# Kernel optimization log

Measured on AMD Instinct MI355X. Metric: run time of the kernel, lower is better.

Reference implementation:

```python
import jax, jax.numpy as jnp
import numpy as np

IMAGE_SIZE = 512
STRIDES = (8, 16, 32)
W_SEG, W_DET, W_CLS = 1.0, 1.0, 0.5


def _bce_logits(x, y):
    # numerically stable binary cross entropy with logits (broadcasts y)
    return jnp.maximum(x, 0.0) - x * y + jnp.log1p(jnp.exp(-jnp.abs(x)))


def _focal_loss_mean(logits, targets, num_classes, alpha=0.25, gamma=2.0):
    # sigmoid focal loss; targets are class indices, -1 (or any negative) => all-background row
    t = jax.nn.one_hot(targets, num_classes, dtype=logits.dtype)
    p = jax.nn.sigmoid(logits)
    ce = _bce_logits(logits, t)
    p_t = p * t + (1.0 - p) * (1.0 - t)
    a_t = alpha * t + (1.0 - alpha) * (1.0 - t)
    return jnp.mean(a_t * (1.0 - p_t) ** gamma * ce)


def _det_scale_loss(cls_logits, reg_preds, cent_preds, boxes, labels, stride):
    B, Cp1, H, W = cls_logits.shape
    C = Cp1 - 1
    L = H * W
    cls = jnp.transpose(cls_logits, (0, 2, 3, 1))[..., 1:].reshape(B, L, C)
    reg = jnp.transpose(reg_preds, (0, 2, 3, 1)).reshape(B, L, 4)
    cent = cent_preds.reshape(B, L)
    xs = (jnp.arange(W, dtype=jnp.float32) + 0.5) * stride
    ys = (jnp.arange(H, dtype=jnp.float32) + 0.5) * stride
    gy, gx = jnp.meshgrid(ys, xs, indexing='ij')
    loc_x = gx.reshape(-1)
    loc_y = gy.reshape(-1)

    def per_image(cls_i, reg_i, cent_i, gb, gl):
        b = gb * IMAGE_SIZE  # [cx,cy,w,h] in pixels
        x0 = b[:, 0] - b[:, 2] * 0.5
        y0 = b[:, 1] - b[:, 3] * 0.5
        x1 = b[:, 0] + b[:, 2] * 0.5
        y1 = b[:, 1] + b[:, 3] * 0.5
        l = loc_x[:, None] - x0[None, :]
        t = loc_y[:, None] - y0[None, :]
        r = x1[None, :] - loc_x[:, None]
        btm = y1[None, :] - loc_y[:, None]
        ltrb = jnp.stack([l, t, r, btm], axis=-1)  # (L, N, 4)
        inside = jnp.min(ltrb, axis=-1) > 0
        area = (x1 - x0) * (y1 - y0)
        masked_area = jnp.where(inside, area[None, :], jnp.inf)
        idx = jnp.argmin(masked_area, axis=-1)  # min-area matched box per location
        pos = jnp.any(inside, axis=-1)
        cls_t = jnp.where(pos, gl[idx], -1)
        reg_t = jnp.take_along_axis(ltrb, idx[:, None, None], axis=1)[:, 0, :] / stride
        lr = reg_t[:, jnp.array([0, 2])]
        tb = reg_t[:, jnp.array([1, 3])]
        eps = 1e-6
        cen_t = jnp.sqrt(jnp.clip((jnp.min(lr, -1) / (jnp.max(lr, -1) + eps)) * (jnp.min(tb, -1) / (jnp.max(tb, -1) + eps)), 0.0, 1.0))
        cls_l = _focal_loss_mean(cls_i, cls_t, C)
        npos = jnp.sum(pos)
        d = reg_i - reg_t
        sl1 = jnp.mean(jnp.where(jnp.abs(d) < 1.0, 0.5 * d * d, jnp.abs(d) - 0.5), axis=-1)
        posf = pos.astype(jnp.float32)
        denom = jnp.maximum(npos, 1).astype(jnp.float32)
        reg_l = jnp.where(npos > 0, jnp.sum(sl1 * posf) / denom, 0.0)
        bce = _bce_logits(cent_i, cen_t)
        cen_l = jnp.where(npos > 0, jnp.sum(bce * posf) / denom, 0.0)
        return cls_l, reg_l, cen_l

    cl, rl, cel = jax.vmap(per_image)(cls, reg, cent, boxes, labels)
    return jnp.mean(cl), jnp.mean(rl), jnp.mean(cel)


def _total_loss(seg_logits, seg_mask, cls_list, reg_list, cen_list, boxes, labels, cls_pred, cls_target):
    # segmentation: BCE-with-logits, integer mask broadcast as float target over channels
    seg_t = seg_mask.astype(jnp.float32)[:, None, :, :]  # (B,1,H,W) broadcasts vs (B,C,H,W)
    seg_loss = jnp.mean(_bce_logits(seg_logits, seg_t))
    tot_cls = 0.0
    tot_reg = 0.0
    tot_cen = 0.0
    for s in range(3):
        cl, rl, cel = _det_scale_loss(cls_list[s], reg_list[s], cen_list[s], boxes, labels, STRIDES[s])
        tot_cls = tot_cls + cl
        tot_reg = tot_reg + rl
        tot_cen = tot_cen + cel
    n = 3.0
    det_loss = tot_cls / n + tot_reg / n + tot_cen / n
    cls_loss = _focal_loss_mean(cls_pred, cls_target, cls_pred.shape[-1])
    return W_SEG * seg_loss + W_DET * det_loss + W_CLS * cls_loss


def setup_inputs() -> dict:
    key = jax.random.key(0)
    ks = jax.random.split(key, 16)
    B = 32
    inp = {
        'seg_logits': jax.random.normal(ks[0], (B, 4, 512, 512), jnp.float32),
        'seg_mask': jax.random.randint(ks[1], (B, 512, 512), 0, 4, jnp.int32),
        'cls_logits_s0': jax.random.normal(ks[2], (B, 5, 64, 64), jnp.float32),
        'cls_logits_s1': jax.random.normal(ks[3], (B, 5, 32, 32), jnp.float32),
        'cls_logits_s2': jax.random.normal(ks[4], (B, 5, 16, 16), jnp.float32),
        'reg_preds_s0': jax.random.normal(ks[5], (B, 4, 64, 64), jnp.float32),
        'reg_preds_s1': jax.random.normal(ks[6], (B, 4, 32, 32), jnp.float32),
        'reg_preds_s2': jax.random.normal(ks[7], (B, 4, 16, 16), jnp.float32),
        'centerness_s0': jax.random.normal(ks[8], (B, 1, 64, 64), jnp.float32),
        'centerness_s1': jax.random.normal(ks[9], (B, 1, 32, 32), jnp.float32),
        'centerness_s2': jax.random.normal(ks[10], (B, 1, 16, 16), jnp.float32),
        'boxes': jax.random.uniform(ks[11], (B, 20, 4), jnp.float32),
        'labels': jax.random.randint(ks[12], (B, 20), 0, 4, jnp.int32),
        'cls_pred': jax.random.normal(ks[13], (B, 10), jnp.float32),
        'cls_target': jax.random.randint(ks[14], (B,), 0, 10, jnp.int32),
    }
    return inp


def reference(seg_logits, seg_mask, cls_logits_s0, cls_logits_s1, cls_logits_s2, reg_preds_s0, reg_preds_s1, reg_preds_s2, centerness_s0, centerness_s1, centerness_s2, boxes, labels, cls_pred, cls_target):
    return _total_loss(seg_logits, seg_mask,
                       (cls_logits_s0, cls_logits_s1, cls_logits_s2),
                       (reg_preds_s0, reg_preds_s1, reg_preds_s2),
                       (centerness_s0, centerness_s1, centerness_s2),
                       boxes, labels, cls_pred, cls_target)
```

## Files before the change

### kernel.cpp

```cpp
#include <hip/hip_runtime.h>
#include <math.h>

#define NB 32
#define SEG_BLOCKS 2048


__device__ __forceinline__ float bce_logits(float x, float y) {
    float a = fabsf(x);
    return fmaxf(x, 0.f) - x * y + __logf(1.f + __expf(-a));
}

__device__ __forceinline__ float focal_elt(float x, float t) {
    float p = 1.f / (1.f + __expf(-x));
    float ce = bce_logits(x, t);
    float p_t = (t > 0.5f) ? p : (1.f - p);
    float a_t = (t > 0.5f) ? 0.25f : 0.75f;
    float om = 1.f - p_t;
    return a_t * om * om * ce;
}

template <int N>
__device__ void blk_reduce_arr(float* v) {
    __shared__ float sm[N][4];
    int lane = threadIdx.x & 63;
    int wid  = threadIdx.x >> 6;
#pragma unroll
    for (int j = 0; j < N; j++) {
        float x = v[j];
#pragma unroll
        for (int off = 32; off > 0; off >>= 1) x += __shfl_down(x, off, 64);
        if (lane == 0) sm[j][wid] = x;
    }
    __syncthreads();
    if (threadIdx.x == 0) {
#pragma unroll
        for (int j = 0; j < N; j++) {
            float s = 0.f;
#pragma unroll
            for (int w = 0; w < 4; w++) s += sm[j][w];
            v[j] = s;
        }
    }
}


__global__ __launch_bounds__(256) void seg_kernel(
        const float* __restrict__ logits, const int* __restrict__ mask,
        float* __restrict__ partial) {
    const int HW  = 512 * 512;
    const int QPI = HW / 4;
    const int TOTQ = NB * QPI;
    int tid = blockIdx.x * 256 + threadIdx.x;
    float acc = 0.f;
    for (int q = tid; q < TOTQ; q += SEG_BLOCKS * 256) {
        int b   = q >> 16;
        int hwq = q & 65535;
        const int4 m4 = ((const int4*)(mask + (size_t)b * HW))[hwq];
        float ty0 = (float)m4.x, ty1 = (float)m4.y, ty2 = (float)m4.z, ty3 = (float)m4.w;
        const float4* base = (const float4*)(logits + (size_t)b * 4 * HW);
#pragma unroll
        for (int c = 0; c < 4; c++) {
            float4 x4 = base[c * QPI + hwq];
            acc += bce_logits(x4.x, ty0) + bce_logits(x4.y, ty1)
                 + bce_logits(x4.z, ty2) + bce_logits(x4.w, ty3);
        }
    }
    float v[1] = {acc};
    blk_reduce_arr<1>(v);
    if (threadIdx.x == 0) partial[blockIdx.x] = v[0];
}


__global__ __launch_bounds__(256) void det_kernel(
        const float* __restrict__ cls0, const float* __restrict__ cls1, const float* __restrict__ cls2,
        const float* __restrict__ reg0, const float* __restrict__ reg1, const float* __restrict__ reg2,
        const float* __restrict__ cen0, const float* __restrict__ cen1, const float* __restrict__ cen2,
        const float* __restrict__ boxes, const int* __restrict__ labels,
        float* __restrict__ outws) {
    const int b = blockIdx.x;
    const int s = blockIdx.y;
    int Wd, shift, L; float stride;
    const float *cls, *reg, *cen;
    if (s == 0)      { Wd = 64; shift = 6; L = 4096; stride = 8.f;  cls = cls0; reg = reg0; cen = cen0; }
    else if (s == 1) { Wd = 32; shift = 5; L = 1024; stride = 16.f; cls = cls1; reg = reg1; cen = cen1; }
    else             { Wd = 16; shift = 4; L = 256;  stride = 32.f; cls = cls2; reg = reg2; cen = cen2; }

    __shared__ float sx0[20], sy0[20], sx1[20], sy1[20], sar[20];
    __shared__ int   slb[20];
    if (threadIdx.x < 20) {
        int k = threadIdx.x;
        const float* bb = boxes + (b * 20 + k) * 4;
        float cx = bb[0] * 512.f, cy = bb[1] * 512.f;
        float w  = bb[2] * 512.f, h  = bb[3] * 512.f;
        float x0 = cx - 0.5f * w, y0 = cy - 0.5f * h;
        float x1 = cx + 0.5f * w, y1 = cy + 0.5f * h;
        sx0[k] = x0; sy0[k] = y0; sx1[k] = x1; sy1[k] = y1;
        sar[k] = (x1 - x0) * (y1 - y0);
        slb[k] = labels[b * 20 + k];
    }
    __syncthreads();

    const float* clsb = cls + (size_t)b * 5 * L;
    const float* regb = reg + (size_t)b * 4 * L;
    const float* cenb = cen + (size_t)b * L;
    const float inv = 1.f / stride;

    float cls_s = 0.f, reg_s = 0.f, cen_s = 0.f, np = 0.f;
    for (int l = threadIdx.x; l < L; l += 256) {
        float lx = ((l & (Wd - 1)) + 0.5f) * stride;
        float ly = ((l >> shift)   + 0.5f) * stride;
        int bk = -1; float ba = INFINITY;
        float bl = 0.f, btp = 0.f, brr = 0.f, bbt = 0.f;
#pragma unroll
        for (int k = 0; k < 20; k++) {
            float li = lx - sx0[k], ti = ly - sy0[k];
            float ri = sx1[k] - lx, bi = sy1[k] - ly;
            float mn = fminf(fminf(li, ti), fminf(ri, bi));
            if (mn > 0.f && sar[k] < ba) {
                ba = sar[k]; bk = k;
                bl = li; btp = ti; brr = ri; bbt = bi;
            }
        }
        int tl = (bk >= 0) ? slb[bk] : -1;
#pragma unroll
        for (int c = 0; c < 4; c++) {
            float x = clsb[(c + 1) * L + l];
            cls_s += focal_elt(x, (c == tl) ? 1.f : 0.f);
        }
        if (bk >= 0) {
            float r0 = bl * inv, r1 = btp * inv, r2 = brr * inv, r3 = bbt * inv;
            float d0 = regb[0 * L + l] - r0;
            float d1 = regb[1 * L + l] - r1;
            float d2 = regb[2 * L + l] - r2;
            float d3 = regb[3 * L + l] - r3;
            float a0 = fabsf(d0), a1 = fabsf(d1), a2 = fabsf(d2), a3 = fabsf(d3);
            float sl = (a0 < 1.f ? 0.5f * d0 * d0 : a0 - 0.5f)
                     + (a1 < 1.f ? 0.5f * d1 * d1 : a1 - 0.5f)
                     + (a2 < 1.f ? 0.5f * d2 * d2 : a2 - 0.5f)
                     + (a3 < 1.f ? 0.5f * d3 * d3 : a3 - 0.5f);
            reg_s += 0.25f * sl;
            float mnlr = fminf(r0, r2), mxlr = fmaxf(r0, r2);
            float mntb = fminf(r1, r3), mxtb = fmaxf(r1, r3);
            float v = (mnlr / (mxlr + 1e-6f)) * (mntb / (mxtb + 1e-6f));
            v = fminf(fmaxf(v, 0.f), 1.f);
            float ct = sqrtf(v);
            cen_s += bce_logits(cenb[l], ct);
            np += 1.f;
        }
    }

    float v4[4] = {cls_s, reg_s, cen_s, np};
    blk_reduce_arr<4>(v4);
    if (threadIdx.x == 0) {
        float* o = outws + (size_t)(s * NB + b) * 4;
        o[0] = v4[0]; o[1] = v4[1]; o[2] = v4[2]; o[3] = v4[3];
    }
}


__global__ __launch_bounds__(256) void final_kernel(
        const float* __restrict__ segpart, const float* __restrict__ detws,
        const float* __restrict__ cls_pred, const int* __restrict__ cls_target,
        float* __restrict__ out) {
    float segs = 0.f;
    for (int i = threadIdx.x; i < SEG_BLOCKS; i += 256) segs += segpart[i];
    float clss = 0.f;
    for (int e = threadIdx.x; e < NB * 10; e += 256) {
        int i = e / 10, c = e - i * 10;
        clss += focal_elt(cls_pred[e], (cls_target[i] == c) ? 1.f : 0.f);
    }
    float v2[2] = {segs, clss};
    blk_reduce_arr<2>(v2);
    if (threadIdx.x == 0) {
        float seg_loss = v2[0] / 33554432.f;
        float cls_loss = v2[1] / 320.f;
        const int Ls[3] = {4096, 1024, 256};
        float tc = 0.f, tr = 0.f, tn = 0.f;
        for (int s = 0; s < 3; s++) {
            float ac = 0.f, ar = 0.f, an = 0.f;
            for (int i = 0; i < NB; i++) {
                const float* o = detws + (size_t)(s * NB + i) * 4;
                ac += o[0] / (Ls[s] * 4.f);
                float np = o[3];
                float denom = fmaxf(np, 1.f);
                if (np > 0.f) {
                    ar += o[1] / denom;
                    an += o[2] / denom;
                }
            }
            tc += ac / (float)NB;
            tr += ar / (float)NB;
            tn += an / (float)NB;
        }
        float det_loss = (tc + tr + tn) / 3.f;
        out[0] = seg_loss + det_loss + 0.5f * cls_loss;
    }
}


extern "C" void kernel_launch(void* const* d_in, const int* in_sizes, int n_in,
                              void* d_out, int out_size, void* d_ws, size_t ws_size,
                              hipStream_t stream) {
    const float* seg_logits = (const float*)d_in[0];
    const int*   seg_mask   = (const int*)d_in[1];
    const float* cls0 = (const float*)d_in[2];
    const float* cls1 = (const float*)d_in[3];
    const float* cls2 = (const float*)d_in[4];
    const float* reg0 = (const float*)d_in[5];
    const float* reg1 = (const float*)d_in[6];
    const float* reg2 = (const float*)d_in[7];
    const float* cen0 = (const float*)d_in[8];
    const float* cen1 = (const float*)d_in[9];
    const float* cen2 = (const float*)d_in[10];
    const float* boxes  = (const float*)d_in[11];
    const int*   labels = (const int*)d_in[12];
    const float* cls_pred   = (const float*)d_in[13];
    const int*   cls_target = (const int*)d_in[14];

    float* ws      = (float*)d_ws;
    float* segpart = ws;
    float* detws   = ws + SEG_BLOCKS;

    seg_kernel<<<SEG_BLOCKS, 256, 0, stream>>>(seg_logits, seg_mask, segpart);
    det_kernel<<<dim3(NB, 3), 256, 0, stream>>>(cls0, cls1, cls2,
                                                reg0, reg1, reg2,
                                                cen0, cen1, cen2,
                                                boxes, labels, detws);
    final_kernel<<<1, 256, 0, stream>>>(segpart, detws, cls_pred, cls_target,
                                        (float*)d_out);
}
```

Measured before the change: 288.2 us.

## Fuse detection loss into segmentation kernel and simplify final reduction

The detection loss work moves into the first 96 blocks of the segmentation kernel. Those blocks also run their share of the segmentation grid-stride loop, so one launch is removed and the small det workload overlaps the bandwidth-bound seg pass. Each det block now computes its normalized per-scale loss directly, which reduces the final kernel to a single scalar block reduction. The cost is extra work and shared-memory pressure on the first blocks, plus a slightly different floating-point summation order.

```diff
diff --git a/kernel.cpp b/kernel.cpp
--- a/kernel.cpp
+++ b/kernel.cpp
@@ -3,6 +3,7 @@
 
 #define NB 32
 #define SEG_BLOCKS 2048
+#define DET_BLOCKS 96
 
 
 __device__ __forceinline__ float bce_logits(float x, float y) {
@@ -44,9 +45,100 @@
 }
 
 
-__global__ __launch_bounds__(256) void seg_kernel(
-        const float* __restrict__ logits, const int* __restrict__ mask,
-        float* __restrict__ partial) {
+__global__ __launch_bounds__(256) void fused_kernel(
+        const float* __restrict__ seg_logits, const int* __restrict__ mask,
+        const float* __restrict__ cls0, const float* __restrict__ cls1, const float* __restrict__ cls2,
+        const float* __restrict__ reg0, const float* __restrict__ reg1, const float* __restrict__ reg2,
+        const float* __restrict__ cen0, const float* __restrict__ cen1, const float* __restrict__ cen2,
+        const float* __restrict__ boxes, const int* __restrict__ labels,
+        float* __restrict__ segpart, float* __restrict__ detc) {
+
+    if (blockIdx.x < DET_BLOCKS) {
+        const int s = blockIdx.x >> 5;
+        const int b = blockIdx.x & 31;
+        int Wd, shift, L; float stride;
+        const float *cls, *reg, *cen;
+        if (s == 0)      { Wd = 64; shift = 6; L = 4096; stride = 8.f;  cls = cls0; reg = reg0; cen = cen0; }
+        else if (s == 1) { Wd = 32; shift = 5; L = 1024; stride = 16.f; cls = cls1; reg = reg1; cen = cen1; }
+        else             { Wd = 16; shift = 4; L = 256;  stride = 32.f; cls = cls2; reg = reg2; cen = cen2; }
+
+        __shared__ float sx0[20], sy0[20], sx1[20], sy1[20], sar[20];
+        __shared__ int   slb[20];
+        if (threadIdx.x < 20) {
+            int k = threadIdx.x;
+            const float* bb = boxes + (b * 20 + k) * 4;
+            float cx = bb[0] * 512.f, cy = bb[1] * 512.f;
+            float w  = bb[2] * 512.f, h  = bb[3] * 512.f;
+            float x0 = cx - 0.5f * w, y0 = cy - 0.5f * h;
+            float x1 = cx + 0.5f * w, y1 = cy + 0.5f * h;
+            sx0[k] = x0; sy0[k] = y0; sx1[k] = x1; sy1[k] = y1;
+            sar[k] = (x1 - x0) * (y1 - y0);
+            slb[k] = labels[b * 20 + k];
+        }
+        __syncthreads();
+
+        const float* clsb = cls + (size_t)b * 5 * L;
+        const float* regb = reg + (size_t)b * 4 * L;
+        const float* cenb = cen + (size_t)b * L;
+        const float inv = 1.f / stride;
+
+        float cls_s = 0.f, reg_s = 0.f, cen_s = 0.f, np = 0.f;
+        for (int l = threadIdx.x; l < L; l += 256) {
+            float lx = ((l & (Wd - 1)) + 0.5f) * stride;
+            float ly = ((l >> shift)   + 0.5f) * stride;
+            int bk = -1; float ba = INFINITY;
+            float bl = 0.f, btp = 0.f, brr = 0.f, bbt = 0.f;
+#pragma unroll
+            for (int k = 0; k < 20; k++) {
+                float li = lx - sx0[k], ti = ly - sy0[k];
+                float ri = sx1[k] - lx, bi = sy1[k] - ly;
+                float mn = fminf(fminf(li, ti), fminf(ri, bi));
+                if (mn > 0.f && sar[k] < ba) {
+                    ba = sar[k]; bk = k;
+                    bl = li; btp = ti; brr = ri; bbt = bi;
+                }
+            }
+            int tl = (bk >= 0) ? slb[bk] : -1;
+#pragma unroll
+            for (int c = 0; c < 4; c++) {
+                float x = clsb[(c + 1) * L + l];
+                cls_s += focal_elt(x, (c == tl) ? 1.f : 0.f);
+            }
+            if (bk >= 0) {
+                float r0 = bl * inv, r1 = btp * inv, r2 = brr * inv, r3 = bbt * inv;
+                float d0 = regb[0 * L + l] - r0;
+                float d1 = regb[1 * L + l] - r1;
+                float d2 = regb[2 * L + l] - r2;
+                float d3 = regb[3 * L + l] - r3;
+                float a0 = fabsf(d0), a1 = fabsf(d1), a2 = fabsf(d2), a3 = fabsf(d3);
+                float sl = (a0 < 1.f ? 0.5f * d0 * d0 : a0 - 0.5f)
+                         + (a1 < 1.f ? 0.5f * d1 * d1 : a1 - 0.5f)
+                         + (a2 < 1.f ? 0.5f * d2 * d2 : a2 - 0.5f)
+                         + (a3 < 1.f ? 0.5f * d3 * d3 : a3 - 0.5f);
+                reg_s += 0.25f * sl;
+                float mnlr = fminf(r0, r2), mxlr = fmaxf(r0, r2);
+                float mntb = fminf(r1, r3), mxtb = fmaxf(r1, r3);
+                float v = (mnlr / (mxlr + 1e-6f)) * (mntb / (mxtb + 1e-6f));
+                v = fminf(fmaxf(v, 0.f), 1.f);
+                float ct = sqrtf(v);
+                cen_s += bce_logits(cenb[l], ct);
+                np += 1.f;
+            }
+        }
+
+        float v4[4] = {cls_s, reg_s, cen_s, np};
+        blk_reduce_arr<4>(v4);
+        if (threadIdx.x == 0) {
+            float cls_l = v4[0] / (L * 4.f);
+            float npos  = v4[3];
+            float denom = fmaxf(npos, 1.f);
+            float reg_l = (npos > 0.f) ? v4[1] / denom : 0.f;
+            float cen_l = (npos > 0.f) ? v4[2] / denom : 0.f;
+            detc[blockIdx.x] = (cls_l + reg_l + cen_l) * (1.f / (float)DET_BLOCKS);
+        }
+        __syncthreads();
+    }
+
     const int HW  = 512 * 512;
     const int QPI = HW / 4;
     const int TOTQ = NB * QPI;
@@ -57,7 +149,7 @@
         int hwq = q & 65535;
         const int4 m4 = ((const int4*)(mask + (size_t)b * HW))[hwq];
         float ty0 = (float)m4.x, ty1 = (float)m4.y, ty2 = (float)m4.z, ty3 = (float)m4.w;
-        const float4* base = (const float4*)(logits + (size_t)b * 4 * HW);
+        const float4* base = (const float4*)(seg_logits + (size_t)b * 4 * HW);
 #pragma unroll
         for (int c = 0; c < 4; c++) {
             float4 x4 = base[c * QPI + hwq];
@@ -67,134 +159,26 @@
     }
     float v[1] = {acc};
     blk_reduce_arr<1>(v);
-    if (threadIdx.x == 0) partial[blockIdx.x] = v[0];
-}
-
-
-__global__ __launch_bounds__(256) void det_kernel(
-        const float* __restrict__ cls0, const float* __restrict__ cls1, const float* __restrict__ cls2,
-        const float* __restrict__ reg0, const float* __restrict__ reg1, const float* __restrict__ reg2,
-        const float* __restrict__ cen0, const float* __restrict__ cen1, const float* __restrict__ cen2,
-        const float* __restrict__ boxes, const int* __restrict__ labels,
-        float* __restrict__ outws) {
-    const int b = blockIdx.x;
-    const int s = blockIdx.y;
-    int Wd, shift, L; float stride;
-    const float *cls, *reg, *cen;
-    if (s == 0)      { Wd = 64; shift = 6; L = 4096; stride = 8.f;  cls = cls0; reg = reg0; cen = cen0; }
-    else if (s == 1) { Wd = 32; shift = 5; L = 1024; stride = 16.f; cls = cls1; reg = reg1; cen = cen1; }
-    else             { Wd = 16; shift = 4; L = 256;  stride = 32.f; cls = cls2; reg = reg2; cen = cen2; }
-
-    __shared__ float sx0[20], sy0[20], sx1[20], sy1[20], sar[20];
-    __shared__ int   slb[20];
-    if (threadIdx.x < 20) {
-        int k = threadIdx.x;
-        const float* bb = boxes + (b * 20 + k) * 4;
-        float cx = bb[0] * 512.f, cy = bb[1] * 512.f;
-        float w  = bb[2] * 512.f, h  = bb[3] * 512.f;
-        float x0 = cx - 0.5f * w, y0 = cy - 0.5f * h;
-        float x1 = cx + 0.5f * w, y1 = cy + 0.5f * h;
-        sx0[k] = x0; sy0[k] = y0; sx1[k] = x1; sy1[k] = y1;
-        sar[k] = (x1 - x0) * (y1 - y0);
-        slb[k] = labels[b * 20 + k];
-    }
-    __syncthreads();
-
-    const float* clsb = cls + (size_t)b * 5 * L;
-    const float* regb = reg + (size_t)b * 4 * L;
-    const float* cenb = cen + (size_t)b * L;
-    const float inv = 1.f / stride;
-
-    float cls_s = 0.f, reg_s = 0.f, cen_s = 0.f, np = 0.f;
-    for (int l = threadIdx.x; l < L; l += 256) {
-        float lx = ((l & (Wd - 1)) + 0.5f) * stride;
-        float ly = ((l >> shift)   + 0.5f) * stride;
-        int bk = -1; float ba = INFINITY;
-        float bl = 0.f, btp = 0.f, brr = 0.f, bbt = 0.f;
-#pragma unroll
-        for (int k = 0; k < 20; k++) {
-            float li = lx - sx0[k], ti = ly - sy0[k];
-            float ri = sx1[k] - lx, bi = sy1[k] - ly;
-            float mn = fminf(fminf(li, ti), fminf(ri, bi));
-            if (mn > 0.f && sar[k] < ba) {
-                ba = sar[k]; bk = k;
-                bl = li; btp = ti; brr = ri; bbt = bi;
-            }
-        }
-        int tl = (bk >= 0) ? slb[bk] : -1;
-#pragma unroll
-        for (int c = 0; c < 4; c++) {
-            float x = clsb[(c + 1) * L + l];
-            cls_s += focal_elt(x, (c == tl) ? 1.f : 0.f);
-        }
-        if (bk >= 0) {
-            float r0 = bl * inv, r1 = btp * inv, r2 = brr * inv, r3 = bbt * inv;
-            float d0 = regb[0 * L + l] - r0;
-            float d1 = regb[1 * L + l] - r1;
-            float d2 = regb[2 * L + l] - r2;
-            float d3 = regb[3 * L + l] - r3;
-            float a0 = fabsf(d0), a1 = fabsf(d1), a2 = fabsf(d2), a3 = fabsf(d3);
-            float sl = (a0 < 1.f ? 0.5f * d0 * d0 : a0 - 0.5f)
-                     + (a1 < 1.f ? 0.5f * d1 * d1 : a1 - 0.5f)
-                     + (a2 < 1.f ? 0.5f * d2 * d2 : a2 - 0.5f)
-                     + (a3 < 1.f ? 0.5f * d3 * d3 : a3 - 0.5f);
-            reg_s += 0.25f * sl;
-            float mnlr = fminf(r0, r2), mxlr = fmaxf(r0, r2);
-            float mntb = fminf(r1, r3), mxtb = fmaxf(r1, r3);
-            float v = (mnlr / (mxlr + 1e-6f)) * (mntb / (mxtb + 1e-6f));
-            v = fminf(fmaxf(v, 0.f), 1.f);
-            float ct = sqrtf(v);
-            cen_s += bce_logits(cenb[l], ct);
-            np += 1.f;
-        }
-    }
-
-    float v4[4] = {cls_s, reg_s, cen_s, np};
-    blk_reduce_arr<4>(v4);
-    if (threadIdx.x == 0) {
-        float* o = outws + (size_t)(s * NB + b) * 4;
-        o[0] = v4[0]; o[1] = v4[1]; o[2] = v4[2]; o[3] = v4[3];
-    }
+    if (threadIdx.x == 0) segpart[blockIdx.x] = v[0];
 }
 
 
 __global__ __launch_bounds__(256) void final_kernel(
-        const float* __restrict__ segpart, const float* __restrict__ detws,
+        const float* __restrict__ segpart, const float* __restrict__ detc,
         const float* __restrict__ cls_pred, const int* __restrict__ cls_target,
         float* __restrict__ out) {
-    float segs = 0.f;
-    for (int i = threadIdx.x; i < SEG_BLOCKS; i += 256) segs += segpart[i];
-    float clss = 0.f;
+    const float seg_scale = 1.f / 33554432.f;
+    const float cls_scale = 0.5f / 320.f;
+    float acc = 0.f;
+    for (int i = threadIdx.x; i < SEG_BLOCKS; i += 256) acc += segpart[i] * seg_scale;
+    if (threadIdx.x < DET_BLOCKS) acc += detc[threadIdx.x];
     for (int e = threadIdx.x; e < NB * 10; e += 256) {
         int i = e / 10, c = e - i * 10;
-        clss += focal_elt(cls_pred[e], (cls_target[i] == c) ? 1.f : 0.f);
-    }
-    float v2[2] = {segs, clss};
-    blk_reduce_arr<2>(v2);
-    if (threadIdx.x == 0) {
-        float seg_loss = v2[0] / 33554432.f;
-        float cls_loss = v2[1] / 320.f;
-        const int Ls[3] = {4096, 1024, 256};
-        float tc = 0.f, tr = 0.f, tn = 0.f;
-        for (int s = 0; s < 3; s++) {
-            float ac = 0.f, ar = 0.f, an = 0.f;
-            for (int i = 0; i < NB; i++) {
-                const float* o = detws + (size_t)(s * NB + i) * 4;
-                ac += o[0] / (Ls[s] * 4.f);
-                float np = o[3];
-                float denom = fmaxf(np, 1.f);
-                if (np > 0.f) {
-                    ar += o[1] / denom;
-                    an += o[2] / denom;
-                }
-            }
-            tc += ac / (float)NB;
-            tr += ar / (float)NB;
-            tn += an / (float)NB;
-        }
-        float det_loss = (tc + tr + tn) / 3.f;
-        out[0] = seg_loss + det_loss + 0.5f * cls_loss;
-    }
+        acc += cls_scale * focal_elt(cls_pred[e], (cls_target[i] == c) ? 1.f : 0.f);
+    }
+    float v[1] = {acc};
+    blk_reduce_arr<1>(v);
+    if (threadIdx.x == 0) out[0] = v[0];
 }
 
 
@@ -219,13 +203,13 @@
 
     float* ws      = (float*)d_ws;
     float* segpart = ws;
-    float* detws   = ws + SEG_BLOCKS;
-
-    seg_kernel<<<SEG_BLOCKS, 256, 0, stream>>>(seg_logits, seg_mask, segpart);
-    det_kernel<<<dim3(NB, 3), 256, 0, stream>>>(cls0, cls1, cls2,
-                                                reg0, reg1, reg2,
-                                                cen0, cen1, cen2,
-                                                boxes, labels, detws);
-    final_kernel<<<1, 256, 0, stream>>>(segpart, detws, cls_pred, cls_target,
+    float* detc    = ws + SEG_BLOCKS;
+
+    fused_kernel<<<SEG_BLOCKS, 256, 0, stream>>>(seg_logits, seg_mask,
+                                                 cls0, cls1, cls2,
+                                                 reg0, reg1, reg2,
+                                                 cen0, cen1, cen2,
+                                                 boxes, labels, segpart, detc);
+    final_kernel<<<1, 256, 0, stream>>>(segpart, detc, cls_pred, cls_target,
                                         (float*)d_out);
 }
```

After: 248.0 us. 14.0% less time.
